# Optimization experiments

Hardware: AMD Instinct MI355X
Metric: run time of the kernel (lower is better)

The kernel has to match this reference:

```python
import jax, jax.numpy as jnp
import numpy as np

S, B, E = 4096, 2, 1024
H = 8
WIN = 256  # one-sided window w; band width = 2*w+1


def _band_scores(q, k_pad, seq_len, band):
    # q: (B,S,H,D), k_pad: (B,S+2w,H,D). Returns (B,S,H,band) banded QK^T.
    def f(o):
        ks = jax.lax.dynamic_slice_in_dim(k_pad, o, seq_len, axis=1)
        return jnp.einsum('bshd,bshd->bsh', q, ks)
    s = jax.lax.map(f, jnp.arange(band))  # (band,B,S,H)
    return jnp.moveaxis(s, 0, -1)          # (B,S,H,band)


def _band_av(probs, v_pad, seq_len, band):
    # probs: (B,S,H,band), v_pad: (B,S+2w,H,D) zero-padded (out-of-range keys
    # contribute zero vectors, matching diagonaled_mm's internal masking).
    bsz, _, heads, _ = probs.shape
    d = v_pad.shape[-1]
    def body(carry, o):
        vs = jax.lax.dynamic_slice_in_dim(v_pad, o, seq_len, axis=1)
        p = jax.lax.dynamic_slice_in_dim(probs, o, 1, axis=3)  # (B,S,H,1)
        return carry + p * vs, None
    init = jnp.zeros((bsz, seq_len, heads, d), probs.dtype)
    out, _ = jax.lax.scan(body, init, jnp.arange(band))
    return out


def setup_inputs() -> dict:
    key = jax.random.key(0)
    ks = jax.random.split(key, 7)
    val = jax.random.normal(ks[0], (S, B, E), dtype=jnp.float32)
    Wq = jax.random.normal(ks[1], (E, E), dtype=jnp.float32) * 0.02
    bq = jax.random.normal(ks[2], (E,), dtype=jnp.float32) * 0.02
    Wk = jax.random.normal(ks[3], (E, E), dtype=jnp.float32) * 0.02
    bk = jax.random.normal(ks[4], (E,), dtype=jnp.float32) * 0.02
    Wv = jax.random.normal(ks[5], (E, E), dtype=jnp.float32) * 0.02
    bv = jax.random.normal(ks[6], (E,), dtype=jnp.float32) * 0.02
    return {"val": val, "Wq": Wq, "bq": bq, "Wk": Wk, "bk": bk, "Wv": Wv, "bv": bv}


def reference(val, Wq, bq, Wk, bk, Wv, bv):
    seq_len, bsz, embed = val.shape
    heads, w = H, WIN
    d = embed // heads
    band = 2 * w + 1
    x = jnp.swapaxes(val, 0, 1)  # (B,S,E), matches val.transpose(0,1)
    scale = 1.0 / np.sqrt(d)
    q = (x @ Wq.T + bq) * scale
    k = x @ Wk.T + bk
    v = x @ Wv.T + bv
    # Faithful to torch: .view(seq_len, bsz, H, D) on a (bsz, seq_len, E)
    # contiguous tensor reinterprets memory (a scramble when B != S), then
    # transpose(0,1). jnp.reshape on row-major matches torch .view exactly.
    mq = jnp.swapaxes(q.reshape(seq_len, bsz, heads, d), 0, 1)  # (B,S,H,D)
    mk = jnp.swapaxes(k.reshape(seq_len, bsz, heads, d), 0, 1)
    mv = jnp.swapaxes(v.reshape(seq_len, bsz, heads, d), 0, 1)
    k_pad = jnp.pad(mk, ((0, 0), (w, w), (0, 0), (0, 0)))  # zero pad => padding=0 scores
    v_pad = jnp.pad(mv, ((0, 0), (w, w), (0, 0), (0, 0)))
    scores = _band_scores(mq, k_pad, seq_len, band)  # (B,S,H,2w+1)
    # No masking before softmax (faithful: padding=0 entries enter softmax as 0)
    probs = jax.nn.softmax(scores, axis=-1)
    # dropout in eval mode (training=False) is identity
    attn = _band_av(probs, v_pad, seq_len, band)  # (B,S,H,D)
    out = jnp.swapaxes(attn, 0, 1).reshape(seq_len, bsz, embed)
    return out
```

## Files before the change

### kernel.cpp

```cpp
#include <hip/hip_runtime.h>
#include <stdint.h>

#define SEQ   4096
#define EMB   1024
#define HD    128
#define WIN   256
#define MROWS 8192

typedef unsigned short u16;
typedef unsigned long long u64;
typedef __bf16 v8bf  __attribute__((ext_vector_type(8)));
typedef float  v4f   __attribute__((ext_vector_type(4)));
typedef u16    v8u16 __attribute__((ext_vector_type(8)));

__device__ __forceinline__ u16 f2bf(float f) {
  uint32_t u = __builtin_bit_cast(uint32_t, f);
  u += 0x7FFFu + ((u >> 16) & 1u);
  return (u16)(u >> 16);
}
__device__ __forceinline__ void gl_lds16(const u16* g, u16* l) {
  __builtin_amdgcn_global_load_lds((const __attribute__((address_space(1))) void*)g,
                                   (__attribute__((address_space(3))) void*)l,
                                   16, 0, 0);
}

__global__ __launch_bounds__(256)
void cvt_f32_bf16(const float* __restrict__ val,
                  const float* __restrict__ Wq,
                  const float* __restrict__ Wk,
                  const float* __restrict__ Wv,
                  u16* __restrict__ valbf, u16* __restrict__ Wbf)
{
  const int seg = blockIdx.y;
  const float* src; u16* dst; int nblk;
  if (seg == 0)      { src = val; dst = valbf;              nblk = 4096; }
  else if (seg == 1) { src = Wq;  dst = Wbf;                nblk = 512;  }
  else if (seg == 2) { src = Wk;  dst = Wbf + (1u << 20);   nblk = 512;  }
  else               { src = Wv;  dst = Wbf + (2u << 20);   nblk = 512;  }
  if ((int)blockIdx.x >= nblk) return;
  const int t = blockIdx.x * 256 + threadIdx.x;
  float4 a = ((const float4*)src)[2 * t];
  float4 b = ((const float4*)src)[2 * t + 1];
  v8u16 o;
  o[0] = f2bf(a.x); o[1] = f2bf(a.y); o[2] = f2bf(a.z); o[3] = f2bf(a.w);
  o[4] = f2bf(b.x); o[5] = f2bf(b.y); o[6] = f2bf(b.z); o[7] = f2bf(b.w);
  ((v8u16*)dst)[t] = o;
}

__global__ __launch_bounds__(256, 3)
void qkv_gemm(const u16* __restrict__ valbf, const u16* __restrict__ Wbf,
              const float* __restrict__ bq, const float* __restrict__ bk,
              const float* __restrict__ bv,
              u16* __restrict__ Qb, u16* __restrict__ Kb, u16* __restrict__ VTg)
{
  __shared__ __align__(16) u16 As[128 * 64];
  __shared__ __align__(16) u16 Bs[128 * 64];

  const int tid  = threadIdx.x;
  const int lane = tid & 63;
  const int w    = tid >> 6;
  const int quad = lane >> 4;
  const int lq   = lane & 15;
  const int wm   = w >> 1, wn = w & 1;

  const int bm = blockIdx.x;
  const int bn = blockIdx.y;

  const int seg = bn >> 3;
  const u16*   Wsel = Wbf + (size_t)seg * EMB * EMB;
  const float* bsel = seg == 0 ? bq : (seg == 1 ? bk : bv);
  const int nseg0 = (bn & 7) * 128;

  const u16* arow[4];
  const u16* brow[4];
#pragma unroll
  for (int call = 0; call < 4; ++call) {
    int c  = call * 256 + w * 64 + lane;
    int m  = c >> 3;
    int qs = c & 7;
    int q  = qs ^ (m & 7);
    int a2 = bm * 128 + m;
    int aa = 2 * (a2 & 4095) + (a2 >> 12);
    int grow = (aa & 4095) * 2 + (aa >> 12);
    arow[call] = valbf + (size_t)grow * EMB + q * 8;
    int n = nseg0 + m;
    brow[call] = Wsel + (size_t)n * EMB + q * 8;
  }

  v4f acc[4][4];
#pragma unroll
  for (int mt = 0; mt < 4; ++mt)
#pragma unroll
    for (int nt = 0; nt < 4; ++nt) acc[mt][nt] = (v4f){0.f, 0.f, 0.f, 0.f};

#pragma unroll 1
  for (int kt = 0; kt < 16; ++kt) {
    const int k0 = kt * 64;
    __syncthreads();
#pragma unroll
    for (int call = 0; call < 4; ++call) {
      gl_lds16(arow[call] + k0, &As[(call * 256 + w * 64) * 8]);
      gl_lds16(brow[call] + k0, &Bs[(call * 256 + w * 64) * 8]);
    }
    __syncthreads();
#pragma unroll
    for (int ks = 0; ks < 2; ++ks) {
      v8bf afr[4], bfr[4];
      const int qa = ks * 4 + quad;
#pragma unroll
      for (int mt = 0; mt < 4; ++mt) {
        int m = wm * 64 + mt * 16 + lq;
        afr[mt] = *(const v8bf*)&As[(m * 8 + (qa ^ (m & 7))) * 8];
      }
#pragma unroll
      for (int nt = 0; nt < 4; ++nt) {
        int n = wn * 64 + nt * 16 + lq;
        bfr[nt] = *(const v8bf*)&Bs[(n * 8 + (qa ^ (n & 7))) * 8];
      }
#pragma unroll
      for (int mt = 0; mt < 4; ++mt)
#pragma unroll
        for (int nt = 0; nt < 4; ++nt)
          acc[mt][nt] = __builtin_amdgcn_mfma_f32_16x16x32_bf16(afr[mt], bfr[nt], acc[mt][nt], 0, 0, 0);
    }
  }

  const float scale = 0.08838834764831845f;
  float bias[4];
#pragma unroll
  for (int nt = 0; nt < 4; ++nt)
    bias[nt] = bsel[nseg0 + wn * 64 + nt * 16 + lq];

  if (seg == 2) {
    const int h  = bn & 7;
    const int bp = bm >> 5;
    const int s0 = (bm & 31) * 128;
#pragma unroll
    for (int mt = 0; mt < 4; ++mt) {
      int mb = wm * 64 + mt * 16 + quad * 4;
#pragma unroll
      for (int nt = 0; nt < 4; ++nt) {
        int n = wn * 64 + nt * 16 + lq;
        u64 pk = 0;
#pragma unroll
        for (int r = 0; r < 4; ++r)
          pk |= (u64)f2bf(acc[mt][nt][r] + bias[nt]) << (16 * r);
        *(u64*)&VTg[((size_t)(bp * 8 + h) * HD + n) * SEQ + s0 + mb] = pk;
      }
    }
  } else {
    u16* Osel = (seg == 0) ? Qb : Kb;
#pragma unroll
    for (int mt = 0; mt < 4; ++mt) {
      int rbase = bm * 128 + wm * 64 + mt * 16 + quad * 4;
#pragma unroll
      for (int nt = 0; nt < 4; ++nt) {
        int ncol = nseg0 + wn * 64 + nt * 16 + lq;
#pragma unroll
        for (int r = 0; r < 4; ++r) {
          float v = acc[mt][nt][r] + bias[nt];
          if (seg == 0) v *= scale;
          Osel[(size_t)(rbase + r) * EMB + ncol] = f2bf(v);
        }
      }
    }
  }
}

__global__ __launch_bounds__(256, 2)
void local_attn(const u16* __restrict__ Qb, const u16* __restrict__ Kb,
                const u16* __restrict__ VTg, float* __restrict__ out)
{
  __shared__ __align__(16) u16 sK [2][64 * 128];
  __shared__ __align__(16) u16 sVT[2][128 * 64];
  __shared__ __align__(16) u16 sP [4][16 * 72];

  const int tid  = threadIdx.x;
  const int lane = tid & 63;
  const int w    = tid >> 6;
  const int quad = lane >> 4;
  const int lq   = lane & 15;

  const int bh = blockIdx.x;
  const int q0 = blockIdx.y * 64;
  const int bp = bh >> 3;
  const int h  = bh & 7;
  const size_t rowbase = (size_t)bp * SEQ;

  const u16* Kbase = Kb + rowbase * EMB + h * HD;
  const u16* Vbase = VTg + (size_t)bh * HD * SEQ;

  v8bf qf[4];
  {
    const u16* qrow = Qb + (rowbase + q0 + w * 16 + lq) * EMB + h * HD;
#pragma unroll
    for (int ks = 0; ks < 4; ++ks)
      qf[ks] = *(const v8bf*)(qrow + ks * 32 + quad * 8);
  }

  v4f oacc[8];
#pragma unroll
  for (int dt = 0; dt < 8; ++dt) oacc[dt] = (v4f){0.f, 0.f, 0.f, 0.f};
  float ls[4] = {0.f, 0.f, 0.f, 0.f};

  const int jlo = (q0 - WIN > 0) ? q0 - WIN : 0;
  const int jhi = (q0 + 64 + WIN < SEQ) ? q0 + 64 + WIN : SEQ;
  const int nit = (jhi - jlo) >> 6;

  auto stage = [&](int kb, int p) {
#pragma unroll
    for (int call = 0; call < 4; ++call) {
      int s = call * 256 + w * 64 + lane;
      int row = s >> 4, sl = s & 15;
      int q = sl ^ (row & 15);
      gl_lds16(Kbase + (size_t)(kb + row) * EMB + q * 8,
               &sK[p][(call * 256 + w * 64) * 8]);
    }
#pragma unroll
    for (int call = 0; call < 4; ++call) {
      int s = call * 256 + w * 64 + lane;
      int d = s >> 3, sl = s & 7;
      int q = sl ^ (d & 7);
      gl_lds16(Vbase + (size_t)d * SEQ + kb + q * 8,
               &sVT[p][(call * 256 + w * 64) * 8]);
    }
  };

  stage(jlo, 0);

#pragma unroll 1
  for (int it = 0; it < nit; ++it) {
    const int p  = it & 1;
    const int kb = jlo + it * 64;
    __syncthreads();
    if (it + 1 < nit) stage(kb + 64, p ^ 1);

    v4f sfr[4];
#pragma unroll
    for (int nt = 0; nt < 4; ++nt) sfr[nt] = (v4f){0.f, 0.f, 0.f, 0.f};
#pragma unroll
    for (int ks = 0; ks < 4; ++ks) {
      const int sl = (ks * 4 + quad) ^ lq;
#pragma unroll
      for (int nt = 0; nt < 4; ++nt) {
        v8bf kf = *(const v8bf*)&sK[p][((nt * 16 + lq) * 16 + sl) * 8];
        sfr[nt] = __builtin_amdgcn_mfma_f32_16x16x32_bf16(qf[ks], kf, sfr[nt], 0, 0, 0);
      }
    }

    const bool need_mask = (kb == q0 - 256) || (kb == q0 + 256);
#pragma unroll
    for (int nt = 0; nt < 4; ++nt) {
#pragma unroll
      for (int r = 0; r < 4; ++r) {
        float pv = __expf(sfr[nt][r]);
        if (need_mask) {
          int j  = kb + nt * 16 + lq;
          int sr = q0 + w * 16 + quad * 4 + r;
          int dd = j - sr;
          pv = (dd <= WIN && dd >= -WIN) ? pv : 0.f;
        }
        ls[r] += pv;
        sP[w][(quad * 4 + r) * 72 + nt * 16 + lq] = f2bf(pv);
      }
    }

#pragma unroll
    for (int kv = 0; kv < 2; ++kv) {
      v8bf pf = *(const v8bf*)&sP[w][lq * 72 + kv * 32 + quad * 8];
      const int slb = (kv * 4 + quad);
#pragma unroll
      for (int dt = 0; dt < 8; ++dt) {
        int d = dt * 16 + lq;
        v8bf vf = *(const v8bf*)&sVT[p][(d * 8 + (slb ^ (d & 7))) * 8];
        oacc[dt] = __builtin_amdgcn_mfma_f32_16x16x32_bf16(pf, vf, oacc[dt], 0, 0, 0);
      }
    }
  }

  float lrow[4];
#pragma unroll
  for (int r = 0; r < 4; ++r) {
    float t = ls[r];
#pragma unroll
    for (int off = 1; off < 16; off <<= 1) t += __shfl_xor(t, off);
    int sr = q0 + w * 16 + quad * 4 + r;
    int npl = WIN - sr;             if (npl < 0) npl = 0;
    int npr = sr - (SEQ - 1 - WIN); if (npr < 0) npr = 0;
    lrow[r] = t + (float)(npl + npr);
  }
#pragma unroll
  for (int dt = 0; dt < 8; ++dt) {
#pragma unroll
    for (int r = 0; r < 4; ++r) {
      int sr = q0 + w * 16 + quad * 4 + r;
      out[(size_t)(2 * sr + bp) * EMB + h * HD + dt * 16 + lq] = oacc[dt][r] / lrow[r];
    }
  }
}

extern "C" void kernel_launch(void* const* d_in, const int* in_sizes, int n_in,
                              void* d_out, int out_size, void* d_ws, size_t ws_size,
                              hipStream_t stream) {
  const float* val = (const float*)d_in[0];
  const float* bq  = (const float*)d_in[2];
  const float* bk  = (const float*)d_in[4];
  const float* bv  = (const float*)d_in[6];
  float* out = (float*)d_out;

  u16* valbf = (u16*)d_ws;
  u16* Wbf   = valbf + (size_t)MROWS * EMB;
  u16* Qb    = Wbf + (size_t)3 * EMB * EMB;
  u16* Kb    = Qb + (size_t)MROWS * EMB;
  u16* VTg   = Kb + (size_t)MROWS * EMB;

  hipLaunchKernelGGL(cvt_f32_bf16, dim3(4096, 4), dim3(256), 0, stream,
                     val, (const float*)d_in[1], (const float*)d_in[3],
                     (const float*)d_in[5], valbf, Wbf);
  hipLaunchKernelGGL(qkv_gemm, dim3(64, 24), dim3(256), 0, stream,
                     valbf, Wbf, bq, bk, bv, Qb, Kb, VTg);
  hipLaunchKernelGGL(local_attn, dim3(16, 64), dim3(256), 0, stream,
                     Qb, Kb, VTg, out);
}
```

Before: 188.7 us.

## Process 128 query rows per attention block to reuse staged K/V tiles

```diff
diff --git a/kernel.cpp b/kernel.cpp
--- a/kernel.cpp
+++ b/kernel.cpp
@@ -182,7 +182,7 @@
   const int lq   = lane & 15;
 
   const int bh = blockIdx.x;
-  const int q0 = blockIdx.y * 64;
+  const int q0 = blockIdx.y * 128;
   const int bp = bh >> 3;
   const int h  = bh & 7;
   const size_t rowbase = (size_t)bp * SEQ;
@@ -190,21 +190,24 @@
   const u16* Kbase = Kb + rowbase * EMB + h * HD;
   const u16* Vbase = VTg + (size_t)bh * HD * SEQ;
 
-  v8bf qf[4];
-  {
-    const u16* qrow = Qb + (rowbase + q0 + w * 16 + lq) * EMB + h * HD;
+  v8bf qf[2][4];
+#pragma unroll
+  for (int mt = 0; mt < 2; ++mt) {
+    const u16* qrow = Qb + (rowbase + q0 + w * 32 + mt * 16 + lq) * EMB + h * HD;
 #pragma unroll
     for (int ks = 0; ks < 4; ++ks)
-      qf[ks] = *(const v8bf*)(qrow + ks * 32 + quad * 8);
-  }
-
-  v4f oacc[8];
-#pragma unroll
-  for (int dt = 0; dt < 8; ++dt) oacc[dt] = (v4f){0.f, 0.f, 0.f, 0.f};
-  float ls[4] = {0.f, 0.f, 0.f, 0.f};
+      qf[mt][ks] = *(const v8bf*)(qrow + ks * 32 + quad * 8);
+  }
+
+  v4f oacc[2][8];
+#pragma unroll
+  for (int mt = 0; mt < 2; ++mt)
+#pragma unroll
+    for (int dt = 0; dt < 8; ++dt) oacc[mt][dt] = (v4f){0.f, 0.f, 0.f, 0.f};
+  float ls[2][4] = {{0.f,0.f,0.f,0.f},{0.f,0.f,0.f,0.f}};
 
   const int jlo = (q0 - WIN > 0) ? q0 - WIN : 0;
-  const int jhi = (q0 + 64 + WIN < SEQ) ? q0 + 64 + WIN : SEQ;
+  const int jhi = (q0 + 128 + WIN < SEQ) ? q0 + 128 + WIN : SEQ;
   const int nit = (jhi - jlo) >> 6;
 
   auto stage = [&](int kb, int p) {
@@ -235,66 +238,79 @@
     __syncthreads();
     if (it + 1 < nit) stage(kb + 64, p ^ 1);
 
-    v4f sfr[4];
-#pragma unroll
-    for (int nt = 0; nt < 4; ++nt) sfr[nt] = (v4f){0.f, 0.f, 0.f, 0.f};
+    v8bf vf[2][8];
+#pragma unroll
+    for (int kv = 0; kv < 2; ++kv)
+#pragma unroll
+      for (int dt = 0; dt < 8; ++dt) {
+        int d = dt * 16 + lq;
+        vf[kv][dt] = *(const v8bf*)&sVT[p][(d * 8 + ((kv * 4 + quad) ^ (d & 7))) * 8];
+      }
+
+    v4f sfr[2][4];
+#pragma unroll
+    for (int mt = 0; mt < 2; ++mt)
+#pragma unroll
+      for (int nt = 0; nt < 4; ++nt) sfr[mt][nt] = (v4f){0.f, 0.f, 0.f, 0.f};
 #pragma unroll
     for (int ks = 0; ks < 4; ++ks) {
       const int sl = (ks * 4 + quad) ^ lq;
 #pragma unroll
       for (int nt = 0; nt < 4; ++nt) {
         v8bf kf = *(const v8bf*)&sK[p][((nt * 16 + lq) * 16 + sl) * 8];
-        sfr[nt] = __builtin_amdgcn_mfma_f32_16x16x32_bf16(qf[ks], kf, sfr[nt], 0, 0, 0);
-      }
-    }
-
-    const bool need_mask = (kb == q0 - 256) || (kb == q0 + 256);
-#pragma unroll
-    for (int nt = 0; nt < 4; ++nt) {
+        sfr[0][nt] = __builtin_amdgcn_mfma_f32_16x16x32_bf16(qf[0][ks], kf, sfr[0][nt], 0, 0, 0);
+        sfr[1][nt] = __builtin_amdgcn_mfma_f32_16x16x32_bf16(qf[1][ks], kf, sfr[1][nt], 0, 0, 0);
+      }
+    }
+
+    const bool need_mask = (kb <= q0 - 192) || (kb >= q0 + 256);
+#pragma unroll
+    for (int mt = 0; mt < 2; ++mt) {
+#pragma unroll
+      for (int nt = 0; nt < 4; ++nt) {
+#pragma unroll
+        for (int r = 0; r < 4; ++r) {
+          float pv = __expf(sfr[mt][nt][r]);
+          if (need_mask) {
+            int j  = kb + nt * 16 + lq;
+            int sr = q0 + w * 32 + mt * 16 + quad * 4 + r;
+            int dd = j - sr;
+            pv = (dd <= WIN && dd >= -WIN) ? pv : 0.f;
+          }
+          ls[mt][r] += pv;
+          sP[w][(quad * 4 + r) * 72 + nt * 16 + lq] = f2bf(pv);
+        }
+      }
+#pragma unroll
+      for (int kv = 0; kv < 2; ++kv) {
+        v8bf pf = *(const v8bf*)&sP[w][lq * 72 + kv * 32 + quad * 8];
+#pragma unroll
+        for (int dt = 0; dt < 8; ++dt)
+          oacc[mt][dt] = __builtin_amdgcn_mfma_f32_16x16x32_bf16(pf, vf[kv][dt], oacc[mt][dt], 0, 0, 0);
+      }
+    }
+  }
+
+#pragma unroll
+  for (int mt = 0; mt < 2; ++mt) {
+    float lrow[4];
+#pragma unroll
+    for (int r = 0; r < 4; ++r) {
+      float t = ls[mt][r];
+#pragma unroll
+      for (int off = 1; off < 16; off <<= 1) t += __shfl_xor(t, off);
+      int sr = q0 + w * 32 + mt * 16 + quad * 4 + r;
+      int npl = WIN - sr;             if (npl < 0) npl = 0;
+      int npr = sr - (SEQ - 1 - WIN); if (npr < 0) npr = 0;
+      lrow[r] = t + (float)(npl + npr);
+    }
+#pragma unroll
+    for (int dt = 0; dt < 8; ++dt) {
 #pragma unroll
       for (int r = 0; r < 4; ++r) {
-        float pv = __expf(sfr[nt][r]);
-        if (need_mask) {
-          int j  = kb + nt * 16 + lq;
-          int sr = q0 + w * 16 + quad * 4 + r;
-          int dd = j - sr;
-          pv = (dd <= WIN && dd >= -WIN) ? pv : 0.f;
-        }
-        ls[r] += pv;
-        sP[w][(quad * 4 + r) * 72 + nt * 16 + lq] = f2bf(pv);
-      }
-    }
-
-#pragma unroll
-    for (int kv = 0; kv < 2; ++kv) {
-      v8bf pf = *(const v8bf*)&sP[w][lq * 72 + kv * 32 + quad * 8];
-      const int slb = (kv * 4 + quad);
-#pragma unroll
-      for (int dt = 0; dt < 8; ++dt) {
-        int d = dt * 16 + lq;
-        v8bf vf = *(const v8bf*)&sVT[p][(d * 8 + (slb ^ (d & 7))) * 8];
-        oacc[dt] = __builtin_amdgcn_mfma_f32_16x16x32_bf16(pf, vf, oacc[dt], 0, 0, 0);
-      }
-    }
-  }
-
-  float lrow[4];
-#pragma unroll
-  for (int r = 0; r < 4; ++r) {
-    float t = ls[r];
-#pragma unroll
-    for (int off = 1; off < 16; off <<= 1) t += __shfl_xor(t, off);
-    int sr = q0 + w * 16 + quad * 4 + r;
-    int npl = WIN - sr;             if (npl < 0) npl = 0;
-    int npr = sr - (SEQ - 1 - WIN); if (npr < 0) npr = 0;
-    lrow[r] = t + (float)(npl + npr);
-  }
-#pragma unroll
-  for (int dt = 0; dt < 8; ++dt) {
-#pragma unroll
-    for (int r = 0; r < 4; ++r) {
-      int sr = q0 + w * 16 + quad * 4 + r;
-      out[(size_t)(2 * sr + bp) * EMB + h * HD + dt * 16 + lq] = oacc[dt][r] / lrow[r];
+        int sr = q0 + w * 32 + mt * 16 + quad * 4 + r;
+        out[(size_t)(2 * sr + bp) * EMB + h * HD + dt * 16 + lq] = oacc[mt][dt][r] / lrow[r];
+      }
     }
   }
 }
@@ -319,6 +335,6 @@
                      (const float*)d_in[5], valbf, Wbf);
   hipLaunchKernelGGL(qkv_gemm, dim3(64, 24), dim3(256), 0, stream,
                      valbf, Wbf, bq, bk, bv, Qb, Kb, VTg);
-  hipLaunchKernelGGL(local_attn, dim3(16, 64), dim3(256), 0, stream,
+  hipLaunchKernelGGL(local_attn, dim3(16, 32), dim3(256), 0, stream,
                      Qb, Kb, VTg, out);
 }
```

After: 191.0 us. No clear change (+1.2%).

## Compute transposed scores so P feeds PV MFMA from registers, drop LDS staging

Applied to the files above, without the earlier changes.

```diff
diff --git a/kernel.cpp b/kernel.cpp
--- a/kernel.cpp
+++ b/kernel.cpp
@@ -12,6 +12,12 @@
 typedef __bf16 v8bf  __attribute__((ext_vector_type(8)));
 typedef float  v4f   __attribute__((ext_vector_type(4)));
 typedef u16    v8u16 __attribute__((ext_vector_type(8)));
+typedef short  v4ss  __attribute__((ext_vector_type(4)));
+
+__device__ __forceinline__ void mfma16(v4f& c, v4ss a, v4ss b) {
+  asm("s_nop 1\n\tv_mfma_f32_16x16x16_bf16 %0, %1, %2, %0"
+      : "+v"(c) : "v"(a), "v"(b));
+}
 
 __device__ __forceinline__ u16 f2bf(float f) {
   uint32_t u = __builtin_bit_cast(uint32_t, f);
@@ -167,13 +173,12 @@
   }
 }
 
-__global__ __launch_bounds__(256, 2)
+__global__ __launch_bounds__(256, 4)
 void local_attn(const u16* __restrict__ Qb, const u16* __restrict__ Kb,
                 const u16* __restrict__ VTg, float* __restrict__ out)
 {
-  __shared__ __align__(16) u16 sK [2][64 * 128];
-  __shared__ __align__(16) u16 sVT[2][128 * 64];
-  __shared__ __align__(16) u16 sP [4][16 * 72];
+  __shared__ __align__(16) u16 sK [64 * 128];
+  __shared__ __align__(16) u16 sVT[128 * 64];
 
   const int tid  = threadIdx.x;
   const int lane = tid & 63;
@@ -198,23 +203,23 @@
       qf[ks] = *(const v8bf*)(qrow + ks * 32 + quad * 8);
   }
 
-  v4f oacc[8];
-#pragma unroll
-  for (int dt = 0; dt < 8; ++dt) oacc[dt] = (v4f){0.f, 0.f, 0.f, 0.f};
-  float ls[4] = {0.f, 0.f, 0.f, 0.f};
+  v4f oaccT[8];
+#pragma unroll
+  for (int dt = 0; dt < 8; ++dt) oaccT[dt] = (v4f){0.f, 0.f, 0.f, 0.f};
+  float ls = 0.f;
 
   const int jlo = (q0 - WIN > 0) ? q0 - WIN : 0;
   const int jhi = (q0 + 64 + WIN < SEQ) ? q0 + 64 + WIN : SEQ;
   const int nit = (jhi - jlo) >> 6;
 
-  auto stage = [&](int kb, int p) {
+  auto stage = [&](int kb) {
 #pragma unroll
     for (int call = 0; call < 4; ++call) {
       int s = call * 256 + w * 64 + lane;
       int row = s >> 4, sl = s & 15;
       int q = sl ^ (row & 15);
       gl_lds16(Kbase + (size_t)(kb + row) * EMB + q * 8,
-               &sK[p][(call * 256 + w * 64) * 8]);
+               &sK[(call * 256 + w * 64) * 8]);
     }
 #pragma unroll
     for (int call = 0; call < 4; ++call) {
@@ -222,79 +227,77 @@
       int d = s >> 3, sl = s & 7;
       int q = sl ^ (d & 7);
       gl_lds16(Vbase + (size_t)d * SEQ + kb + q * 8,
-               &sVT[p][(call * 256 + w * 64) * 8]);
+               &sVT[(call * 256 + w * 64) * 8]);
     }
   };
-
-  stage(jlo, 0);
 
 #pragma unroll 1
   for (int it = 0; it < nit; ++it) {
-    const int p  = it & 1;
     const int kb = jlo + it * 64;
+    stage(kb);
     __syncthreads();
-    if (it + 1 < nit) stage(kb + 64, p ^ 1);
-
-    v4f sfr[4];
-#pragma unroll
-    for (int nt = 0; nt < 4; ++nt) sfr[nt] = (v4f){0.f, 0.f, 0.f, 0.f};
+
+    v4f st[4];
+#pragma unroll
+    for (int nt = 0; nt < 4; ++nt) st[nt] = (v4f){0.f, 0.f, 0.f, 0.f};
 #pragma unroll
     for (int ks = 0; ks < 4; ++ks) {
       const int sl = (ks * 4 + quad) ^ lq;
 #pragma unroll
       for (int nt = 0; nt < 4; ++nt) {
-        v8bf kf = *(const v8bf*)&sK[p][((nt * 16 + lq) * 16 + sl) * 8];
-        sfr[nt] = __builtin_amdgcn_mfma_f32_16x16x32_bf16(qf[ks], kf, sfr[nt], 0, 0, 0);
+        v8bf kf = *(const v8bf*)&sK[((nt * 16 + lq) * 16 + sl) * 8];
+        st[nt] = __builtin_amdgcn_mfma_f32_16x16x32_bf16(kf, qf[ks], st[nt], 0, 0, 0);
       }
     }
 
     const bool need_mask = (kb == q0 - 256) || (kb == q0 + 256);
+    v4ss pf[4];
 #pragma unroll
     for (int nt = 0; nt < 4; ++nt) {
 #pragma unroll
       for (int r = 0; r < 4; ++r) {
-        float pv = __expf(sfr[nt][r]);
+        float pv = __expf(st[nt][r]);
         if (need_mask) {
-          int j  = kb + nt * 16 + lq;
-          int sr = q0 + w * 16 + quad * 4 + r;
+          int j  = kb + nt * 16 + quad * 4 + r;
+          int sr = q0 + w * 16 + lq;
           int dd = j - sr;
           pv = (dd <= WIN && dd >= -WIN) ? pv : 0.f;
         }
-        ls[r] += pv;
-        sP[w][(quad * 4 + r) * 72 + nt * 16 + lq] = f2bf(pv);
-      }
-    }
-
-#pragma unroll
-    for (int kv = 0; kv < 2; ++kv) {
-      v8bf pf = *(const v8bf*)&sP[w][lq * 72 + kv * 32 + quad * 8];
-      const int slb = (kv * 4 + quad);
+        ls += pv;
+        pf[nt][r] = (short)f2bf(pv);
+      }
+    }
+
+#pragma unroll
+    for (int nt = 0; nt < 4; ++nt) {
 #pragma unroll
       for (int dt = 0; dt < 8; ++dt) {
         int d = dt * 16 + lq;
-        v8bf vf = *(const v8bf*)&sVT[p][(d * 8 + (slb ^ (d & 7))) * 8];
-        oacc[dt] = __builtin_amdgcn_mfma_f32_16x16x32_bf16(pf, vf, oacc[dt], 0, 0, 0);
-      }
-    }
-  }
-
-  float lrow[4];
-#pragma unroll
-  for (int r = 0; r < 4; ++r) {
-    float t = ls[r];
-#pragma unroll
-    for (int off = 1; off < 16; off <<= 1) t += __shfl_xor(t, off);
-    int sr = q0 + w * 16 + quad * 4 + r;
+        int slot = (nt * 2 + (quad >> 1)) ^ (d & 7);
+        v4ss vt = *(const v4ss*)&sVT[(d * 8 + slot) * 8 + (quad & 1) * 4];
+        mfma16(oaccT[dt], vt, pf[nt]);
+      }
+    }
+    __syncthreads();
+  }
+
+  asm volatile("s_nop 7\n\ts_nop 7");
+
+  {
+    float t = ls;
+    t += __shfl_xor(t, 16);
+    t += __shfl_xor(t, 32);
+    const int sr = q0 + w * 16 + lq;
     int npl = WIN - sr;             if (npl < 0) npl = 0;
     int npr = sr - (SEQ - 1 - WIN); if (npr < 0) npr = 0;
-    lrow[r] = t + (float)(npl + npr);
-  }
-#pragma unroll
-  for (int dt = 0; dt < 8; ++dt) {
-#pragma unroll
-    for (int r = 0; r < 4; ++r) {
-      int sr = q0 + w * 16 + quad * 4 + r;
-      out[(size_t)(2 * sr + bp) * EMB + h * HD + dt * 16 + lq] = oacc[dt][r] / lrow[r];
+    const float inv = 1.0f / (t + (float)(npl + npr));
+    float* orow = out + (size_t)(2 * sr + bp) * EMB + h * HD;
+#pragma unroll
+    for (int dt = 0; dt < 8; ++dt) {
+      v4f o;
+#pragma unroll
+      for (int r = 0; r < 4; ++r) o[r] = oaccT[dt][r] * inv;
+      *(v4f*)(orow + dt * 16 + quad * 4) = o;
     }
   }
 }
```

Measured after the change: 187.8 us. No clear change (-0.5%).
